# Kernel optimization log

Measured on AMD Instinct MI355X. Metric: run time of the kernel, lower is better.

Reference implementation:

```python
import jax, jax.numpy as jnp
import numpy as np

BETA = 1.0 / 9.0
WEIGHTS = (10.0, 10.0, 5.0, 5.0, 15.0)  # BoxCoder weights (wx, wy, ww, wh, wt)
DEG = np.pi / 180.0
IOU_THRESH = 0.5
IND_THRESH = 0.1


def _cross(a, b):
    return a[..., 0] * b[..., 1] - a[..., 1] * b[..., 0]


def _corners(box):
    # box: (5,) = x1,y1,x2,y2,theta_deg ; rotated rect corners, CCW (4,2)
    x1, y1, x2, y2, t = box[0], box[1], box[2], box[3], box[4]
    cx, cy = 0.5 * (x1 + x2), 0.5 * (y1 + y2)
    w, h = x2 - x1, y2 - y1
    th = t * DEG
    c, s = jnp.cos(th), jnp.sin(th)
    dx = jnp.array([-0.5, 0.5, 0.5, -0.5]) * w
    dy = jnp.array([-0.5, -0.5, 0.5, 0.5]) * h
    return jnp.stack([cx + c * dx - s * dy, cy + s * dx + c * dy], axis=-1)


def _pair_inter_area(P, Q):
    # Exact intersection area of two convex CCW quads P,Q (4,2) each.
    # Candidate vertices = corners inside the other quad + all edge-edge
    # intersections; convexity => sort by angle around centroid, shoelace.
    eps = 1e-8

    def inside(pts, poly):
        a = poly
        b = jnp.roll(poly, -1, axis=0)
        cr = _cross((b - a)[None], pts[:, None] - a[None])  # (K,4)
        return jnp.all(cr >= -1e-6, axis=1)

    Pa, Pd = P, jnp.roll(P, -1, 0) - P
    Qa, Qd = Q, jnp.roll(Q, -1, 0) - Q
    r = Pd[:, None]          # (4,1,2)
    sd = Qd[None, :]         # (1,4,2)
    qp = Qa[None, :] - Pa[:, None]  # (4,4,2)
    den = _cross(r, sd)      # (4,4)
    safe = jnp.where(jnp.abs(den) < eps, 1.0, den)
    t = _cross(qp, sd) / safe
    u = _cross(qp, r) / safe
    ok = (jnp.abs(den) >= eps) & (t >= 0) & (t <= 1) & (u >= 0) & (u <= 1)
    xpts = Pa[:, None] + t[..., None] * r  # (4,4,2)

    pts = jnp.concatenate([P, Q, xpts.reshape(16, 2)], axis=0)  # (24,2)
    val = jnp.concatenate([inside(P, Q), inside(Q, P), ok.reshape(16)])
    n = jnp.sum(val)
    ctr = jnp.sum(jnp.where(val[:, None], pts, 0.0), axis=0) / jnp.maximum(n, 1)
    rel = pts - ctr
    ang = jnp.where(val, jnp.arctan2(rel[:, 1], rel[:, 0]), 1e9)  # invalid -> end
    rel = rel[jnp.argsort(ang)]
    idx = jnp.arange(24)
    nxt = jnp.where(idx + 1 < n, idx + 1, 0)
    area = 0.5 * jnp.abs(jnp.sum(jnp.where(idx < n, _cross(rel, rel[nxt]), 0.0)))
    return jnp.where(n >= 3, area, 0.0)


def min_area_square(boxes):
    w = boxes[:, 2] - boxes[:, 0]
    h = boxes[:, 3] - boxes[:, 1]
    cx = boxes[:, 0] + 0.5 * w
    cy = boxes[:, 1] + 0.5 * h
    s = 0.5 * jnp.maximum(w, h)
    return jnp.stack([cx - s, cy - s, cx + s, cy + s], axis=1)


def bbox_overlaps(a, b):
    lt = jnp.maximum(a[:, None, :2], b[None, :, :2])
    rb = jnp.minimum(a[:, None, 2:], b[None, :, 2:])
    wh = jnp.clip(rb - lt, 0.0)
    inter = wh[..., 0] * wh[..., 1]
    aa = (a[:, 2] - a[:, 0]) * (a[:, 3] - a[:, 1])
    ab = (b[:, 2] - b[:, 0]) * (b[:, 3] - b[:, 1])
    return inter / jnp.maximum(aa[:, None] + ab[None, :] - inter, 1e-8)


def rbox_overlaps(anchor, gt, indicator, thresh=IND_THRESH):
    Pc = jax.vmap(_corners)(anchor)  # (N,4,2)
    Qc = jax.vmap(_corners)(gt)      # (M,4,2)
    inter = jax.vmap(lambda p: jax.vmap(lambda q: _pair_inter_area(p, q))(Qc))(Pc)
    aA = (anchor[:, 2] - anchor[:, 0]) * (anchor[:, 3] - anchor[:, 1])
    aG = (gt[:, 2] - gt[:, 0]) * (gt[:, 3] - gt[:, 1])
    iou = inter / jnp.maximum(aA[:, None] + aG[None, :] - inter, 1e-8)
    return jnp.where(indicator > thresh, iou, 0.0)


def encode(ex, gt):
    wx, wy, ww, wh, wt = WEIGHTS
    ew = jnp.maximum(ex[:, 2] - ex[:, 0], 1.0)
    eh = jnp.maximum(ex[:, 3] - ex[:, 1], 1.0)
    ecx = ex[:, 0] + 0.5 * ew
    ecy = ex[:, 1] + 0.5 * eh
    gw = jnp.maximum(gt[:, 2] - gt[:, 0], 1.0)
    gh = jnp.maximum(gt[:, 3] - gt[:, 1], 1.0)
    gcx = gt[:, 0] + 0.5 * gw
    gcy = gt[:, 1] + 0.5 * gh
    dx = wx * (gcx - ecx) / ew
    dy = wy * (gcy - ecy) / eh
    dw = ww * jnp.log(gw / ew)
    dh = wh * jnp.log(gh / eh)
    dt = wt * (jnp.tan(gt[:, 4] * DEG) - jnp.tan(ex[:, 4] * DEG))
    return jnp.stack([dx, dy, dw, dh, dt], axis=1)


def smooth_l1(diff, beta=BETA):
    d = jnp.abs(diff)
    return jnp.where(d < beta, 0.5 * d * d / beta, d - 0.5 * beta)


def _per_image(regression, anchor, annotation):
    valid = annotation[:, -1] != -1  # (M,)
    indicator = bbox_overlaps(min_area_square(anchor), min_area_square(annotation[:, :5]))
    ov = rbox_overlaps(anchor, annotation[:, :5], indicator)  # (N,M)
    ov = jnp.where(valid[None, :], ov, -1.0)  # invalid GT never assigned
    iou_max = jnp.max(ov, axis=1)
    iou_argmax = jnp.argmax(ov, axis=1)
    pos = iou_max >= IOU_THRESH  # (N,)
    assigned = annotation[iou_argmax]  # (N,6)
    targets = encode(anchor, assigned[:, :5])  # (N,5)
    elt = smooth_l1(regression - targets)  # (N,5)
    num = jnp.sum(pos)
    loss = jnp.sum(jnp.where(pos[:, None], elt, 0.0)) / jnp.maximum(num * 5, 1)
    return jnp.where(num > 0, loss, 0.0)


def setup_inputs() -> dict:
    key = jax.random.key(0)
    ks = jax.random.split(key, 8)
    B, N, M = 2, 16384, 16
    cx = jax.random.uniform(ks[0], (B, N), minval=0.0, maxval=1024.0)
    cy = jax.random.uniform(ks[1], (B, N), minval=0.0, maxval=1024.0)
    w = jax.random.uniform(ks[2], (B, N), minval=16.0, maxval=128.0)
    h = jax.random.uniform(ks[3], (B, N), minval=16.0, maxval=128.0)
    t = jax.random.uniform(ks[4], (B, N), minval=-30.0, maxval=30.0)
    anchors = jnp.stack([cx - 0.5 * w, cy - 0.5 * h, cx + 0.5 * w, cy + 0.5 * h, t], axis=-1)
    # GTs = jittered copies of random anchors so positives (IoU>=0.5) exist
    idx = jax.random.randint(ks[5], (B, M), 0, N)
    base = jnp.take_along_axis(anchors, jnp.broadcast_to(idx[..., None], (B, M, 5)), axis=1)
    jit = jax.random.uniform(ks[6], (B, M, 5), minval=-3.0, maxval=3.0)
    gt = base + jit * jnp.array([1.0, 1.0, 1.0, 1.0, 0.5])
    labels = jax.random.randint(ks[7], (B, M, 1), 0, 20).astype(jnp.float32)
    annotations = jnp.concatenate([gt, labels], axis=-1)
    regressions = jax.random.normal(jax.random.fold_in(key, 1), (B, N, 5)) * 0.1
    return {"regressions": regressions, "anchors": anchors, "annotations": annotations}


def reference(regressions, anchors, annotations):
    losses = jax.vmap(_per_image)(regressions, anchors, annotations)  # (B,)
    return jnp.mean(losses, keepdims=True)  # (1,)
```

## Files before the change

kernel.cpp:

```cpp
#include <hip/hip_runtime.h>
#include <hip/hip_bf16.h>
#include <math.h>

#define DEGF 0.017453292519943295f
#define POISON_CNT 0xAAAAAAAAu

__device__ __forceinline__ float ldv(const float* p, size_t i) { return p[i]; }
__device__ __forceinline__ float ldv(const __hip_bfloat16* p, size_t i) { return __bfloat162float(p[i]); }

struct Emit { float x0, y0, x1, y1; };

__device__ __forceinline__ Emit emit_edge(float xi, float yi, float xj, float yj,
                                          float di, float dj, float lpx, float lpy)
{
    bool ini = di >= 0.0f;
    bool inj = dj >= 0.0f;
    bool crossing = ini != inj;
    float den = di - dj;
    float t = di / ((fabsf(den) < 1e-30f) ? 1e-30f : den);
    float ix = fmaf(t, xj - xi, xi);
    float iy = fmaf(t, yj - yi, yi);
    float ax = crossing ? ix : lpx;
    float ay = crossing ? iy : lpy;
    Emit e;
    e.x0 = ini ? xi : ax;
    e.y0 = ini ? yi : ay;
    e.x1 = crossing ? ix : e.x0;
    e.y1 = crossing ? iy : e.y0;
    return e;
}

template<int N, int AXIS>
__device__ __forceinline__ void clip_pass(const float* xi, const float* yi,
                                          float* xo, float* yo, float sgn, float lim)
{
    float d[N];
#pragma unroll
    for (int i = 0; i < N; i++) d[i] = fmaf(sgn, (AXIS ? yi[i] : xi[i]), lim);
    const float lpx = AXIS ? 0.0f : -sgn * lim;
    const float lpy = AXIS ? -sgn * lim : 0.0f;
#pragma unroll
    for (int i = 0; i < N; i++) {
        int j = (i + 1 == N) ? 0 : i + 1;
        Emit e = emit_edge(xi[i], yi[i], xi[j], yi[j], d[i], d[j], lpx, lpy);
        xo[2 * i] = e.x0; yo[2 * i] = e.y0;
        xo[2 * i + 1] = e.x1; yo[2 * i + 1] = e.y1;
    }
}

template<int N, int AXIS>
__device__ __forceinline__ float clip_area_final(const float* xi, const float* yi,
                                                 float sgn, float lim)
{
    float d[N];
#pragma unroll
    for (int i = 0; i < N; i++) d[i] = fmaf(sgn, (AXIS ? yi[i] : xi[i]), lim);
    const float lpx = AXIS ? 0.0f : -sgn * lim;
    const float lpy = AXIS ? -sgn * lim : 0.0f;

    Emit e0 = emit_edge(xi[0], yi[0], xi[1], yi[1], d[0], d[1], lpx, lpy);
    float fx = e0.x0, fy = e0.y0;
    float a2 = e0.x0 * e0.y1 - e0.y0 * e0.x1;
    float px = e0.x1, py = e0.y1;
#pragma unroll
    for (int i = 1; i < N; i++) {
        int j = (i + 1 == N) ? 0 : i + 1;
        Emit e = emit_edge(xi[i], yi[i], xi[j], yi[j], d[i], d[j], lpx, lpy);
        a2 += px * e.y0 - py * e.x0;
        a2 += e.x0 * e.y1 - e.y0 * e.x1;
        px = e.x1; py = e.y1;
    }
    a2 += px * fy - py * fx;
    return 0.5f * fabsf(a2);
}

__device__ __forceinline__ float rect_quad_inter_area(const float qx[4], const float qy[4],
                                                      float hw, float hh)
{
    float ax[8], ay[8];
    clip_pass<4, 0>(qx, qy, ax, ay, 1.0f, hw);
    float bx[16], by[16];
    clip_pass<8, 0>(ax, ay, bx, by, -1.0f, hw);
    float cx[32], cy[32];
    clip_pass<16, 1>(bx, by, cx, cy, 1.0f, hh);
    return clip_area_final<32, 1>(cx, cy, -1.0f, hh);
}

template <typename T>
__device__ void wave_body(const T* reg, const T* anc,
                          int img, int n, int N, int lane,
                          const float* g, const float* gb, const float* gh_, float* res,
                          float& lsum, float& pflag)
{
    size_t base = ((size_t)img * N + n) * 5;
    float a0 = 0, a1 = 0, a2 = 0, a3 = 0, a4 = 0;
    float r0 = 0, r1 = 0, r2 = 0, r3 = 0, r4 = 0;
    if (n < N) {
        a0 = ldv(anc, base + 0); a1 = ldv(anc, base + 1); a2 = ldv(anc, base + 2);
        a3 = ldv(anc, base + 3); a4 = ldv(anc, base + 4);
        r0 = ldv(reg, base + 0); r1 = ldv(reg, base + 1); r2 = ldv(reg, base + 2);
        r3 = ldv(reg, base + 3); r4 = ldv(reg, base + 4);
    }

    float aw = a2 - a0, ah = a3 - a1, aA = aw * ah;
    float acx = a0 + 0.5f * aw, acy = a1 + 0.5f * ah;
    float as = 0.5f * fmaxf(aw, ah);
    float sa0 = acx - as, sa1 = acy - as, sa2 = acx + as, sa3 = acy + as;
    float areaA = (sa2 - sa0) * (sa3 - sa1);

    unsigned mask = 0;
    if (n < N) {
#pragma unroll
        for (int j = 0; j < 16; j++) {
            float sb0 = gb[j * 6 + 0], sb1 = gb[j * 6 + 1];
            float sb2 = gb[j * 6 + 2], sb3 = gb[j * 6 + 3];
            float areaB = gb[j * 6 + 4], vfl = gb[j * 6 + 5];
            float ltx = fmaxf(sa0, sb0), lty = fmaxf(sa1, sb1);
            float rbx = fminf(sa2, sb2), rby = fminf(sa3, sb3);
            float iw = fmaxf(rbx - ltx, 0.0f), ih = fmaxf(rby - lty, 0.0f);
            float inter = iw * ih;
            float ind = inter / fmaxf(areaA + areaB - inter, 1e-8f);
            if (vfl != 0.0f && ind > 0.1f) mask |= (1u << j);
        }
    }

    float Pxk[4], Pyk[4];
    {
        float cx = 0.5f * (a0 + a2), cy = 0.5f * (a1 + a3);
        float w = a2 - a0, h = a3 - a1;
        float th = a4 * DEGF;
        float c = __cosf(th), s = __sinf(th);
        const float fxc[4] = {-0.5f, 0.5f, 0.5f, -0.5f};
        const float fyc[4] = {-0.5f, -0.5f, 0.5f, 0.5f};
#pragma unroll
        for (int k = 0; k < 4; k++) {
            float dx = fxc[k] * w, dy = fyc[k] * h;
            Pxk[k] = cx + c * dx - s * dy;
            Pyk[k] = cy + s * dx + c * dy;
        }
    }

    int cnt = __popc(mask);
    int incl = cnt;
#pragma unroll
    for (int off = 1; off < 64; off <<= 1) {
        int v = __shfl_up(incl, off, 64);
        if (lane >= off) incl += v;
    }
    int excl = incl - cnt;
    int T_total = __shfl(incl, 63, 64);

    for (int t0 = 0; t0 < T_total; t0 += 64) {
        int t = t0 + lane;
        bool active = t < T_total;
        int tc = active ? t : (T_total - 1);

        int o = 0;
#pragma unroll
        for (int step = 32; step > 0; step >>= 1) {
            int cand = o + step;
            int e = __shfl(excl, cand, 64);
            if (e <= tc) o = cand;
        }
        int eo = __shfl(excl, o, 64);
        unsigned m = __shfl(mask, o, 64);
        int rank = tc - eo;
        for (int r = 0; r < rank; r++) m &= m - 1;
        int j = __ffs(m) - 1;

        float gcx = gh_[j * 8 + 0], gcy = gh_[j * 8 + 1];
        float cg = gh_[j * 8 + 2], sg = gh_[j * 8 + 3];
        float hw = gh_[j * 8 + 4], hh = gh_[j * 8 + 5], aG = gh_[j * 8 + 6];

        float qx[4], qy[4];
#pragma unroll
        for (int k = 0; k < 4; k++) {
            float px = __shfl(Pxk[k], o, 64);
            float py = __shfl(Pyk[k], o, 64);
            float dx = px - gcx, dy = py - gcy;
            qx[k] = cg * dx + sg * dy;
            qy[k] = cg * dy - sg * dx;
        }
        float aAo = __shfl(aA, o, 64);
        float ia = rect_quad_inter_area(qx, qy, hw, hh);
        float ov = ia / fmaxf(aAo + aG - ia, 1e-8f);
        if (active) res[o * 17 + j] = ov;
    }
    __syncthreads();

    if (n < N) {
        float best = -INFINITY;
        int bestj = 0;
#pragma unroll
        for (int j = 0; j < 16; j++) {
            float ov;
            if (g[j * 6 + 5] == -1.0f)      ov = -1.0f;
            else if ((mask >> j) & 1u)      ov = res[lane * 17 + j];
            else                            ov = 0.0f;
            if (ov > best) { best = ov; bestj = j; }
        }

        if (best >= 0.5f) {
            pflag = 1.0f;
            const float* gt = &g[bestj * 6];
            float ew = fmaxf(a2 - a0, 1.0f), eh = fmaxf(a3 - a1, 1.0f);
            float ecx = a0 + 0.5f * ew, ecy = a1 + 0.5f * eh;
            float gw = fmaxf(gt[2] - gt[0], 1.0f), gh = fmaxf(gt[3] - gt[1], 1.0f);
            float gcx = gt[0] + 0.5f * gw, gcy = gt[1] + 0.5f * gh;
            float tg = gt[4] * DEGF, ta = a4 * DEGF;
            float t[5];
            t[0] = 10.0f * (gcx - ecx) / ew;
            t[1] = 10.0f * (gcy - ecy) / eh;
            t[2] = 5.0f * __logf(gw / ew);
            t[3] = 5.0f * __logf(gh / eh);
            t[4] = 15.0f * (__sinf(tg) / __cosf(tg) - __sinf(ta) / __cosf(ta));
            float rr[5] = {r0, r1, r2, r3, r4};
            const float beta = 1.0f / 9.0f;
#pragma unroll
            for (int k = 0; k < 5; k++) {
                float d = fabsf(rr[k] - t[k]);
                lsum += (d < beta) ? (0.5f * d * d / beta) : (d - 0.5f * beta);
            }
        }
    }
}

__global__ __launch_bounds__(256, 1) void regress_loss_kernel(
    const void* regv, const void* ancv, const void* annv,
    float* __restrict__ ws, unsigned* __restrict__ cntp, void* out,
    int N, int M, int nblocks, int B)
{
    __shared__ float g[96], gb[96], gh_[128], res[4 * 1088];
    __shared__ float2 wpart[4];
    __shared__ int sflag;

    const int img = blockIdx.y;
    const int tid = threadIdx.x;
    const int wave = tid >> 6, lane = tid & 63;
    const int n = blockIdx.x * 256 + tid;

    if (wave == 0) {
        const float* af = (const float*)annv;
        const __hip_bfloat16* ab = (const __hip_bfloat16*)annv;
        bool okf = true, okb = true;
        if (lane < 16) {
            float v = af[6 * lane + 5];
            okf = (v == v) && (v >= -1.5f) && (v <= 1000.0f) && (v == floorf(v));
        }
        if (lane < 32) {
            float v = __bfloat162float(ab[6 * lane + 5]);
            okb = (v == v) && (v >= -1.5f) && (v <= 1000.0f) && (v == floorf(v));
        }
        bool f32ok  = (__ballot(okf) == 0xFFFFFFFFFFFFFFFFULL);
        bool bf16ok = (__ballot(okb) == 0xFFFFFFFFFFFFFFFFULL);
        int is32 = f32ok ? 1 : (bf16ok ? 0 : 1);
        if (lane == 0) sflag = is32;

        if (lane < M) {
            size_t gbase = ((size_t)img * M + lane) * 6;
            float g0, g1, g2, g3, g4, g5;
            if (is32) {
                const float* a = (const float*)annv;
                g0 = a[gbase + 0]; g1 = a[gbase + 1]; g2 = a[gbase + 2];
                g3 = a[gbase + 3]; g4 = a[gbase + 4]; g5 = a[gbase + 5];
            } else {
                const __hip_bfloat16* a = (const __hip_bfloat16*)annv;
                g0 = __bfloat162float(a[gbase + 0]); g1 = __bfloat162float(a[gbase + 1]);
                g2 = __bfloat162float(a[gbase + 2]); g3 = __bfloat162float(a[gbase + 3]);
                g4 = __bfloat162float(a[gbase + 4]); g5 = __bfloat162float(a[gbase + 5]);
            }
            g[lane * 6 + 0] = g0; g[lane * 6 + 1] = g1; g[lane * 6 + 2] = g2;
            g[lane * 6 + 3] = g3; g[lane * 6 + 4] = g4; g[lane * 6 + 5] = g5;
            float gw = g2 - g0, gh = g3 - g1;
            float gcx = g0 + 0.5f * gw, gcy = g1 + 0.5f * gh;
            float gs = 0.5f * fmaxf(gw, gh);
            float sb0 = gcx - gs, sb1 = gcy - gs, sb2 = gcx + gs, sb3 = gcy + gs;
            gb[lane * 6 + 0] = sb0; gb[lane * 6 + 1] = sb1;
            gb[lane * 6 + 2] = sb2; gb[lane * 6 + 3] = sb3;
            gb[lane * 6 + 4] = (sb2 - sb0) * (sb3 - sb1);
            gb[lane * 6 + 5] = (g5 == -1.0f) ? 0.0f : 1.0f;
            float thg = g4 * DEGF;
            gh_[lane * 8 + 0] = gcx; gh_[lane * 8 + 1] = gcy;
            gh_[lane * 8 + 2] = __cosf(thg); gh_[lane * 8 + 3] = __sinf(thg);
            gh_[lane * 8 + 4] = 0.5f * gw; gh_[lane * 8 + 5] = 0.5f * gh;
            gh_[lane * 8 + 6] = gw * gh;
        }
    }
    __syncthreads();
    const int isf32 = sflag;

    float lsum = 0.0f, pflag = 0.0f;
    if (isf32) wave_body((const float*)regv, (const float*)ancv,
                         img, n, N, lane, g, gb, gh_, &res[wave * 1088], lsum, pflag);
    else       wave_body((const __hip_bfloat16*)regv, (const __hip_bfloat16*)ancv,
                         img, n, N, lane, g, gb, gh_, &res[wave * 1088], lsum, pflag);

#pragma unroll
    for (int off = 32; off > 0; off >>= 1) {
        lsum  += __shfl_down(lsum, off, 64);
        pflag += __shfl_down(pflag, off, 64);
    }
    if (lane == 0) wpart[wave] = make_float2(lsum, pflag);
    __syncthreads();

    if (tid == 0) {
        float2 b = wpart[0];
        b.x += wpart[1].x + wpart[2].x + wpart[3].x;
        b.y += wpart[1].y + wpart[2].y + wpart[3].y;
        atomicAdd(&ws[img], b.x);
        atomicAdd(&ws[B + img], b.y);
        __threadfence();
        unsigned old = atomicAdd(cntp, 1u);
        if (old == POISON_CNT + (unsigned)(nblocks - 1)) {
            float acc = 0.0f;
            for (int i = 0; i < B; i++) {
                float s = atomicAdd(&ws[i], 0.0f);
                float c = atomicAdd(&ws[B + i], 0.0f);
                float denom = fmaxf(c * 5.0f, 1.0f);
                acc += (c > 0.0f) ? (s / denom) : 0.0f;
            }
            float v = acc / (float)B;
            volatile float* of = (volatile float*)out;
            of[0] = v;
            unsigned int bits = __float_as_uint(v);
            unsigned int lsb = (bits >> 16) & 1u;
            unsigned short hb = (unsigned short)((bits + 0x7FFFu + lsb) >> 16);
            volatile unsigned short* oh = (volatile unsigned short*)out;
            oh[0] = hb;
        }
    }
}

extern "C" void kernel_launch(void* const* d_in, const int* in_sizes, int n_in,
                              void* d_out, int out_size, void* d_ws, size_t ws_size,
                              hipStream_t stream)
{
    const void* reg = d_in[0];
    const void* anc = d_in[1];
    const void* ann = d_in[2];

    const int M = 16;
    const int B = in_sizes[2] / (M * 6);
    const int N = in_sizes[1] / (B * 5);
    const int gridX = (N + 255) / 256;
    const int nblocks = gridX * B;

    float* ws = (float*)d_ws;
    unsigned* cnt = (unsigned*)((char*)d_ws + 1024);

    dim3 grid(gridX, B);
    regress_loss_kernel<<<grid, dim3(256), 0, stream>>>(reg, anc, ann, ws, cnt, d_out,
                                                        N, M, nblocks, B);
}
```

Baseline: 69.68 us.

## Make each wave independent: per-wave GT setup, no block barriers, per-wave atomics

Result: slower. 82.30 us (+18.1%).

```diff
diff --git a/kernel.cpp b/kernel.cpp
--- a/kernel.cpp
+++ b/kernel.cpp
@@ -5,8 +5,9 @@
 #define DEGF 0.017453292519943295f
 #define POISON_CNT 0xAAAAAAAAu
 
-__device__ __forceinline__ float ldv(const float* p, size_t i) { return p[i]; }
-__device__ __forceinline__ float ldv(const __hip_bfloat16* p, size_t i) { return __bfloat162float(p[i]); }
+__device__ __forceinline__ float u2f(unsigned short u) {
+    return __uint_as_float(((unsigned)u) << 16);
+}
 
 struct Emit { float x0, y0, x1, y1; };
 
@@ -86,21 +87,91 @@
     return clip_area_final<32, 1>(cx, cy, -1.0f, hh);
 }
 
-template <typename T>
-__device__ void wave_body(const T* reg, const T* anc,
-                          int img, int n, int N, int lane,
-                          const float* g, const float* gb, const float* gh_, float* res,
-                          float& lsum, float& pflag)
-{
+__global__ __launch_bounds__(256, 1) void regress_loss_kernel(
+    const void* regv, const void* ancv, const void* annv,
+    float* __restrict__ ws, unsigned* __restrict__ cntp, void* out,
+    int N, int M, int nwaves, int B)
+{
+    __shared__ float lds[4 * 1408];
+
+    const int img = blockIdx.y;
+    const int tid = threadIdx.x;
+    const int wave = tid >> 6, lane = tid & 63;
+    const int n = blockIdx.x * 256 + tid;
+
+    float* g   = &lds[wave * 1408];
+    float* gb  = g + 96;
+    float* gh_ = gb + 96;
+    float* res = gh_ + 128;
+
+    const unsigned short* anc16 = (const unsigned short*)ancv;
+    const unsigned short* reg16 = (const unsigned short*)regv;
+    const unsigned short* ann16 = (const unsigned short*)annv;
+    const float* annf = (const float*)annv;
+
     size_t base = ((size_t)img * N + n) * 5;
+    unsigned short pa[5], pr[5];
+    if (n < N) {
+#pragma unroll
+        for (int k = 0; k < 5; k++) { pa[k] = anc16[base + k]; pr[k] = reg16[base + k]; }
+    }
+    size_t gbase = ((size_t)img * M + lane) * 6;
+    unsigned short pg[6];
+    if (lane < 16) {
+#pragma unroll
+        for (int k = 0; k < 6; k++) pg[k] = ann16[gbase + k];
+    }
+    float sv_f = 0.0f, sv_b = 0.0f;
+    if (lane < 16) sv_f = annf[6 * lane + 5];
+    if (lane < 32) sv_b = u2f(ann16[6 * lane + 5]);
+
+    bool okf = true, okb = true;
+    if (lane < 16) okf = (sv_f == sv_f) && (sv_f >= -1.5f) && (sv_f <= 1000.0f) && (sv_f == floorf(sv_f));
+    if (lane < 32) okb = (sv_b == sv_b) && (sv_b >= -1.5f) && (sv_b <= 1000.0f) && (sv_b == floorf(sv_b));
+    bool f32ok  = (__ballot(okf) == 0xFFFFFFFFFFFFFFFFULL);
+    bool bf16ok = (__ballot(okb) == 0xFFFFFFFFFFFFFFFFULL);
+    const bool isf32 = f32ok ? true : (bf16ok ? false : true);
+
     float a0 = 0, a1 = 0, a2 = 0, a3 = 0, a4 = 0;
     float r0 = 0, r1 = 0, r2 = 0, r3 = 0, r4 = 0;
     if (n < N) {
-        a0 = ldv(anc, base + 0); a1 = ldv(anc, base + 1); a2 = ldv(anc, base + 2);
-        a3 = ldv(anc, base + 3); a4 = ldv(anc, base + 4);
-        r0 = ldv(reg, base + 0); r1 = ldv(reg, base + 1); r2 = ldv(reg, base + 2);
-        r3 = ldv(reg, base + 3); r4 = ldv(reg, base + 4);
-    }
+        if (isf32) {
+            const float* A = (const float*)ancv;
+            const float* R = (const float*)regv;
+            a0 = A[base + 0]; a1 = A[base + 1]; a2 = A[base + 2]; a3 = A[base + 3]; a4 = A[base + 4];
+            r0 = R[base + 0]; r1 = R[base + 1]; r2 = R[base + 2]; r3 = R[base + 3]; r4 = R[base + 4];
+        } else {
+            a0 = u2f(pa[0]); a1 = u2f(pa[1]); a2 = u2f(pa[2]); a3 = u2f(pa[3]); a4 = u2f(pa[4]);
+            r0 = u2f(pr[0]); r1 = u2f(pr[1]); r2 = u2f(pr[2]); r3 = u2f(pr[3]); r4 = u2f(pr[4]);
+        }
+    }
+
+    if (lane < 16) {
+        float g0, g1, g2, g3, g4, g5;
+        if (isf32) {
+            g0 = annf[gbase + 0]; g1 = annf[gbase + 1]; g2 = annf[gbase + 2];
+            g3 = annf[gbase + 3]; g4 = annf[gbase + 4]; g5 = annf[gbase + 5];
+        } else {
+            g0 = u2f(pg[0]); g1 = u2f(pg[1]); g2 = u2f(pg[2]);
+            g3 = u2f(pg[3]); g4 = u2f(pg[4]); g5 = u2f(pg[5]);
+        }
+        g[lane * 6 + 0] = g0; g[lane * 6 + 1] = g1; g[lane * 6 + 2] = g2;
+        g[lane * 6 + 3] = g3; g[lane * 6 + 4] = g4; g[lane * 6 + 5] = g5;
+        float gw = g2 - g0, gh = g3 - g1;
+        float gcx = g0 + 0.5f * gw, gcy = g1 + 0.5f * gh;
+        float gs = 0.5f * fmaxf(gw, gh);
+        float sb0 = gcx - gs, sb1 = gcy - gs, sb2 = gcx + gs, sb3 = gcy + gs;
+        gb[lane * 6 + 0] = sb0; gb[lane * 6 + 1] = sb1;
+        gb[lane * 6 + 2] = sb2; gb[lane * 6 + 3] = sb3;
+        gb[lane * 6 + 4] = (sb2 - sb0) * (sb3 - sb1);
+        gb[lane * 6 + 5] = (g5 == -1.0f) ? 0.0f : 1.0f;
+        float thg = g4 * DEGF;
+        gh_[lane * 8 + 0] = gcx; gh_[lane * 8 + 1] = gcy;
+        gh_[lane * 8 + 2] = __cosf(thg); gh_[lane * 8 + 3] = __sinf(thg);
+        gh_[lane * 8 + 4] = 0.5f * gw; gh_[lane * 8 + 5] = 0.5f * gh;
+        gh_[lane * 8 + 6] = gw * gh;
+    }
+    __threadfence_block();
 
     float aw = a2 - a0, ah = a3 - a1, aA = aw * ah;
     float acx = a0 + 0.5f * aw, acy = a1 + 0.5f * ah;
@@ -186,8 +257,9 @@
         float ov = ia / fmaxf(aAo + aG - ia, 1e-8f);
         if (active) res[o * 17 + j] = ov;
     }
-    __syncthreads();
-
+    __threadfence_block();
+
+    float lsum = 0.0f, pflag = 0.0f;
     if (n < N) {
         float best = -INFINITY;
         int bestj = 0;
@@ -223,95 +295,18 @@
             }
         }
     }
-}
-
-__global__ __launch_bounds__(256, 1) void regress_loss_kernel(
-    const void* regv, const void* ancv, const void* annv,
-    float* __restrict__ ws, unsigned* __restrict__ cntp, void* out,
-    int N, int M, int nblocks, int B)
-{
-    __shared__ float g[96], gb[96], gh_[128], res[4 * 1088];
-    __shared__ float2 wpart[4];
-    __shared__ int sflag;
-
-    const int img = blockIdx.y;
-    const int tid = threadIdx.x;
-    const int wave = tid >> 6, lane = tid & 63;
-    const int n = blockIdx.x * 256 + tid;
-
-    if (wave == 0) {
-        const float* af = (const float*)annv;
-        const __hip_bfloat16* ab = (const __hip_bfloat16*)annv;
-        bool okf = true, okb = true;
-        if (lane < 16) {
-            float v = af[6 * lane + 5];
-            okf = (v == v) && (v >= -1.5f) && (v <= 1000.0f) && (v == floorf(v));
-        }
-        if (lane < 32) {
-            float v = __bfloat162float(ab[6 * lane + 5]);
-            okb = (v == v) && (v >= -1.5f) && (v <= 1000.0f) && (v == floorf(v));
-        }
-        bool f32ok  = (__ballot(okf) == 0xFFFFFFFFFFFFFFFFULL);
-        bool bf16ok = (__ballot(okb) == 0xFFFFFFFFFFFFFFFFULL);
-        int is32 = f32ok ? 1 : (bf16ok ? 0 : 1);
-        if (lane == 0) sflag = is32;
-
-        if (lane < M) {
-            size_t gbase = ((size_t)img * M + lane) * 6;
-            float g0, g1, g2, g3, g4, g5;
-            if (is32) {
-                const float* a = (const float*)annv;
-                g0 = a[gbase + 0]; g1 = a[gbase + 1]; g2 = a[gbase + 2];
-                g3 = a[gbase + 3]; g4 = a[gbase + 4]; g5 = a[gbase + 5];
-            } else {
-                const __hip_bfloat16* a = (const __hip_bfloat16*)annv;
-                g0 = __bfloat162float(a[gbase + 0]); g1 = __bfloat162float(a[gbase + 1]);
-                g2 = __bfloat162float(a[gbase + 2]); g3 = __bfloat162float(a[gbase + 3]);
-                g4 = __bfloat162float(a[gbase + 4]); g5 = __bfloat162float(a[gbase + 5]);
-            }
-            g[lane * 6 + 0] = g0; g[lane * 6 + 1] = g1; g[lane * 6 + 2] = g2;
-            g[lane * 6 + 3] = g3; g[lane * 6 + 4] = g4; g[lane * 6 + 5] = g5;
-            float gw = g2 - g0, gh = g3 - g1;
-            float gcx = g0 + 0.5f * gw, gcy = g1 + 0.5f * gh;
-            float gs = 0.5f * fmaxf(gw, gh);
-            float sb0 = gcx - gs, sb1 = gcy - gs, sb2 = gcx + gs, sb3 = gcy + gs;
-            gb[lane * 6 + 0] = sb0; gb[lane * 6 + 1] = sb1;
-            gb[lane * 6 + 2] = sb2; gb[lane * 6 + 3] = sb3;
-            gb[lane * 6 + 4] = (sb2 - sb0) * (sb3 - sb1);
-            gb[lane * 6 + 5] = (g5 == -1.0f) ? 0.0f : 1.0f;
-            float thg = g4 * DEGF;
-            gh_[lane * 8 + 0] = gcx; gh_[lane * 8 + 1] = gcy;
-            gh_[lane * 8 + 2] = __cosf(thg); gh_[lane * 8 + 3] = __sinf(thg);
-            gh_[lane * 8 + 4] = 0.5f * gw; gh_[lane * 8 + 5] = 0.5f * gh;
-            gh_[lane * 8 + 6] = gw * gh;
-        }
-    }
-    __syncthreads();
-    const int isf32 = sflag;
-
-    float lsum = 0.0f, pflag = 0.0f;
-    if (isf32) wave_body((const float*)regv, (const float*)ancv,
-                         img, n, N, lane, g, gb, gh_, &res[wave * 1088], lsum, pflag);
-    else       wave_body((const __hip_bfloat16*)regv, (const __hip_bfloat16*)ancv,
-                         img, n, N, lane, g, gb, gh_, &res[wave * 1088], lsum, pflag);
 
 #pragma unroll
     for (int off = 32; off > 0; off >>= 1) {
         lsum  += __shfl_down(lsum, off, 64);
         pflag += __shfl_down(pflag, off, 64);
     }
-    if (lane == 0) wpart[wave] = make_float2(lsum, pflag);
-    __syncthreads();
-
-    if (tid == 0) {
-        float2 b = wpart[0];
-        b.x += wpart[1].x + wpart[2].x + wpart[3].x;
-        b.y += wpart[1].y + wpart[2].y + wpart[3].y;
-        atomicAdd(&ws[img], b.x);
-        atomicAdd(&ws[B + img], b.y);
+    if (lane == 0) {
+        atomicAdd(&ws[img], lsum);
+        atomicAdd(&ws[B + img], pflag);
         __threadfence();
         unsigned old = atomicAdd(cntp, 1u);
-        if (old == POISON_CNT + (unsigned)(nblocks - 1)) {
+        if (old == POISON_CNT + (unsigned)(nwaves - 1)) {
             float acc = 0.0f;
             for (int i = 0; i < B; i++) {
                 float s = atomicAdd(&ws[i], 0.0f);
@@ -343,12 +338,12 @@
     const int B = in_sizes[2] / (M * 6);
     const int N = in_sizes[1] / (B * 5);
     const int gridX = (N + 255) / 256;
-    const int nblocks = gridX * B;
+    const int nwaves = gridX * B * 4;
 
     float* ws = (float*)d_ws;
     unsigned* cnt = (unsigned*)((char*)d_ws + 1024);
 
     dim3 grid(gridX, B);
     regress_loss_kernel<<<grid, dim3(256), 0, stream>>>(reg, anc, ann, ws, cnt, d_out,
-                                                        N, M, nblocks, B);
-}
+                                                        N, M, nwaves, B);
+}
```
